# Kernel tuning notes

Hardware: AMD Instinct MI355X
Metric: run time of the kernel (lower is better)

Reference implementation:

```python
import jax, jax.numpy as jnp
import numpy as np

IGNORE = 255
THRESH = 0.7
MIN_KEPT = 100000
AUX_W = 1.0


def resize_bilinear_ac(x, oh, ow):
    # F.interpolate(..., mode='bilinear', align_corners=True); x: (b,c,h,w)
    b, c, h, w = x.shape
    ys = jnp.linspace(0.0, h - 1.0, oh)
    xs = jnp.linspace(0.0, w - 1.0, ow)
    y0 = jnp.floor(ys).astype(jnp.int32)
    x0 = jnp.floor(xs).astype(jnp.int32)
    y1 = jnp.minimum(y0 + 1, h - 1)
    x1 = jnp.minimum(x0 + 1, w - 1)
    wy = (ys - y0)[:, None]          # (oh,1) broadcasts over (b,c,oh,w)
    wx = xs - x0                     # (ow,)
    rows = x[:, :, y0, :] * (1.0 - wy) + x[:, :, y1, :] * wy   # (b,c,oh,w)
    return rows[:, :, :, x0] * (1.0 - wx) + rows[:, :, :, x1] * wx


def ohem_ce(pred, target):
    # pred: (b,c,h,w) logits, target: (b,h,w) int labels
    b, c, h, w = pred.shape
    n = b * h * w
    t = target.reshape(-1)
    valid = t != IGNORE
    t_cl = jnp.where(valid, t, 0)
    logits = pred.transpose(0, 2, 3, 1).reshape(n, c)
    logp = jax.nn.log_softmax(logits, axis=-1)
    pix = jnp.arange(n)
    logp_t = logp[pix, t_cl]
    # prob at target class; invalid pixels filled with 1 (as in masked_fill_)
    mask_prob = jnp.where(valid, jnp.exp(logp_t), 1.0)
    idx = min(n, MIN_KEPT) - 1
    thr = jnp.maximum(jnp.asarray(THRESH, pred.dtype), jnp.sort(mask_prob)[idx])
    kept = mask_prob <= thr
    final_valid = valid & kept
    nll = -logp_t
    denom = jnp.maximum(final_valid.sum(), 1).astype(pred.dtype)
    return jnp.sum(jnp.where(final_valid, nll, 0.0)) / denom


def boundary_bce(p, t):
    # p: (n,1,h,w) probs, t: (n,1,h,w) binary targets; per-sample pos/neg weights
    pos = jnp.sum(t == 1.0, axis=(1, 2, 3), keepdims=True).astype(p.dtype)
    neg = jnp.sum(t == 0.0, axis=(1, 2, 3), keepdims=True).astype(p.dtype)
    valid = pos + neg
    wgt = jnp.where(t == 1.0, neg / valid, jnp.where(t == 0.0, pos / valid, 0.0))
    logp = jnp.clip(jnp.log(p), -100.0)          # torch BCELoss clamps log at -100
    log1mp = jnp.clip(jnp.log(1.0 - p), -100.0)
    bce = -(t * logp + (1.0 - t) * log1mp)
    return jnp.mean(wgt * bce)


def setup_inputs() -> dict:
    key = jax.random.key(0)
    k1, k2, k3, k4, k5 = jax.random.split(key, 5)
    main_pred = jax.random.normal(k1, (4, 19, 64, 128), dtype=jnp.float32)
    coarse_pred = jax.random.normal(k2, (4, 19, 64, 128), dtype=jnp.float32)
    boundary_pred = jax.random.uniform(k3, (4, 1, 64, 128), dtype=jnp.float32)
    seg_gt = jax.random.randint(k4, (4, 512, 1024), 0, 19, dtype=jnp.int32)
    boundary_gt = jax.random.randint(k5, (4, 1, 512, 1024), 0, 2).astype(jnp.float32)
    return {"main_pred": main_pred, "coarse_pred": coarse_pred,
            "boundary_pred": boundary_pred, "seg_gt": seg_gt,
            "boundary_gt": boundary_gt}


def reference(main_pred, coarse_pred, boundary_pred, seg_gt, boundary_gt):
    h, w = seg_gt.shape[1], seg_gt.shape[2]
    main_up = resize_bilinear_ac(main_pred, h, w)
    loss = ohem_ce(main_up, seg_gt)
    coarse_up = resize_bilinear_ac(coarse_pred, h, w)
    loss = loss + AUX_W * ohem_ce(coarse_up, seg_gt)
    bound_up = resize_bilinear_ac(boundary_pred, h, w)
    loss = loss + boundary_bce(bound_up, boundary_gt)
    return loss
```

## Files before the change

### kernel.cpp

```cpp
#include <hip/hip_runtime.h>

#define NPX    2097152
#define NPX4   (NPX/4)
#define CH_STR 8192
#define IMG_STR 155648

#define OFF_CTL   (2ull*NPX*4)
#define CTL_HIST    0
#define CTL_BAR     24576
#define CTL_PREFIX  24578
#define CTL_KREM    24580
#define CTL_THR     24582
#define CTL_PPSUM   24584
#define CTL_PPCNT   28680
#define CTL_OPSUM   32776
#define CTL_OPCNT   33288
#define CTL_BPS     33800
#define CTL_BPC     34824

__global__ __launch_bounds__(256) void fused_pass1(
    const float* __restrict__ mp, const float* __restrict__ cp,
    const float* __restrict__ bp, const int* __restrict__ seg,
    const float* __restrict__ bg,
    float* __restrict__ probA, float* __restrict__ ppsum, unsigned* __restrict__ ppcnt,
    float* __restrict__ bps, unsigned* __restrict__ bpc, unsigned* __restrict__ bar)
{
    __shared__ float2 erow[19 * 128];
    __shared__ float rf[4]; __shared__ unsigned ru[4];
    __shared__ float rf2[4]; __shared__ unsigned ru2[4];
    int bk = blockIdx.x;
    int tid = threadIdx.x;

    if (bk == 0 && tid < 2) bar[tid] = 0u;

    if (bk < 4096) {
        int head = bk >> 11;
        int task = bk & 2047;
        int b = task >> 9;
        int y = task & 511;
        const float* pred = head ? cp : mp;

        float fy = (float)y * (63.0f / 511.0f);
        int y0 = min((int)fy, 63);
        int y1 = min(y0 + 1, 63);
        float wy = fy - (float)y0;

        const float* r0 = pred + (size_t)b * IMG_STR + y0 * 128;
        const float* r1 = pred + (size_t)b * IMG_STR + y1 * 128;
        for (int i = tid; i < 2432; i += 256) {
            int c = i >> 7, x = i & 127;
            float v0 = r0[c * CH_STR + x];
            float v1 = r1[c * CH_STR + x];
            float e = fmaf(wy, v1 - v0, v0);
            erow[c * 128 + x].x = e;
            if (x > 0)    erow[c * 128 + x - 1].y = e;
            if (x == 127) erow[c * 128 + 127].y = e;
        }
        __syncthreads();

        int xb = tid << 2;
        int P = (b * 512 + y) * 1024 + xb;
        int4 t4 = *(const int4*)(seg + P);
        int t[4] = {t4.x, t4.y, t4.z, t4.w};

        float fx0 = (float)xb * (127.0f / 1023.0f);
        int X = min((int)fx0, 126);
        float wA[4], wB[4], wC[4];
#pragma unroll
        for (int dx = 0; dx < 4; ++dx) {
            float fx = (float)(xb + dx) * (127.0f / 1023.0f);
            int x0 = min((int)fx, 127);
            float wx = fx - (float)x0;
            bool sm = (x0 == X);
            wA[dx] = sm ? (1.0f - wx) : 0.0f;
            wB[dx] = sm ? wx : (1.0f - wx);
            wC[dx] = sm ? 0.0f : wx;
        }

        float s[4] = {0.f, 0.f, 0.f, 0.f};
        for (int c = 0; c < 19; ++c) {
            float2 eA = erow[c * 128 + X];
            float2 eB = erow[c * 128 + X + 1];
#pragma unroll
            for (int dx = 0; dx < 4; ++dx) {
                float l = fmaf(eA.x, wA[dx], fmaf(eA.y, wB[dx], eB.y * wC[dx]));
                s[dx] += __expf(l);
            }
        }

        float fs = 0.f; unsigned ic = 0;
        float pr[4];
#pragma unroll
        for (int dx = 0; dx < 4; ++dx) {
            bool valid = (t[dx] != 255);
            int tc = valid ? t[dx] : 0;
            float2 eA = erow[tc * 128 + X];
            float2 eB = erow[tc * 128 + X + 1];
            float lt = fmaf(eA.x, wA[dx], fmaf(eA.y, wB[dx], eB.y * wC[dx]));
            float ls = __logf(s[dx]);
            float n  = ls - lt;
            float p  = fminf(__expf(-n), 1.0f);
            pr[dx] = valid ? p : 1.0f;
            if (valid && p <= 0.7f) { fs += n; ic++; }
        }
        *(float4*)(probA + (size_t)head * NPX + P) = make_float4(pr[0], pr[1], pr[2], pr[3]);

        for (int o = 32; o; o >>= 1) {
            fs += __shfl_down(fs, o, 64);
            ic += (unsigned)__shfl_down((int)ic, o, 64);
        }
        int wave = tid >> 6, lane = tid & 63;
        if (lane == 0) { rf[wave] = fs; ru[wave] = ic; }
        __syncthreads();
        if (tid == 0) {
            ppsum[head * 2048 + task] = rf[0] + rf[1] + rf[2] + rf[3];
            ppcnt[head * 2048 + task] = ru[0] + ru[1] + ru[2] + ru[3];
        }
    } else {
        int bb = bk - 4096;
        int b  = bb >> 7;
        int blk = bb & 127;
        float psum = 0.f, nsum = 0.f; unsigned pc = 0, nc = 0;

        for (int g = blk * 256 + tid; g < 131072; g += 128 * 256) {
            int P = g << 2;
            int y = P >> 10, xb = P & 1023;

            float fy = (float)y * (63.0f / 511.0f);
            int y0 = min((int)fy, 63);
            int y1 = min(y0 + 1, 63);
            float wy = fy - (float)y0;

            const float* r0 = bp + b * 8192 + y0 * 128;
            const float* r1 = bp + b * 8192 + y1 * 128;
            float fx0 = (float)xb * (127.0f / 1023.0f);
            int X  = min((int)fx0, 126);
            int X2 = min(X + 2, 127);
            float c0 = r0[X], c1 = r0[X + 1], c2 = r0[X2];
            float d0 = r1[X], d1 = r1[X + 1], d2 = r1[X2];
            float e0 = fmaf(wy, d0 - c0, c0);
            float e1 = fmaf(wy, d1 - c1, c1);
            float e2 = fmaf(wy, d2 - c2, c2);

            float4 t4 = *(const float4*)(bg + (size_t)b * 524288 + P);
            float tv[4] = {t4.x, t4.y, t4.z, t4.w};

#pragma unroll
            for (int dx = 0; dx < 4; ++dx) {
                float fx = (float)(xb + dx) * (127.0f / 1023.0f);
                int x0 = min((int)fx, 127);
                int x1 = min(x0 + 1, 127);
                float wx = fx - (float)x0;
                float a0 = (x0 == X)     ? e0 : e1;
                float a1 = (x1 == X + 1) ? e1 : e2;
                float p  = fmaf(wx, a1 - a0, a0);
                bool isp = (tv[dx] == 1.0f);
                bool isn = (tv[dx] == 0.0f);
                float q = isp ? p : 1.0f - p;
                float l = fmaxf(__logf(q), -100.0f);
                if (isp) { pc++; psum -= l; }
                if (isn) { nc++; nsum -= l; }
            }
        }
        for (int o = 32; o; o >>= 1) {
            psum += __shfl_down(psum, o, 64);
            nsum += __shfl_down(nsum, o, 64);
            pc   += (unsigned)__shfl_down((int)pc, o, 64);
            nc   += (unsigned)__shfl_down((int)nc, o, 64);
        }
        int wave = tid >> 6, lane = tid & 63;
        if (lane == 0) { rf[wave] = psum; rf2[wave] = nsum; ru[wave] = pc; ru2[wave] = nc; }
        __syncthreads();
        if (tid == 0) {
            bps[2 * bb]     = rf[0] + rf[1] + rf[2] + rf[3];
            bps[2 * bb + 1] = rf2[0] + rf2[1] + rf2[2] + rf2[3];
            bpc[2 * bb]     = ru[0] + ru[1] + ru[2] + ru[3];
            bpc[2 * bb + 1] = ru2[0] + ru2[1] + ru2[2] + ru2[3];
        }
    }
}

__device__ __forceinline__ void gbar(unsigned* bar, int tid) {
    __syncthreads();
    if (tid == 0) {
        unsigned g = __hip_atomic_load(&bar[1], __ATOMIC_RELAXED, __HIP_MEMORY_SCOPE_AGENT);
        unsigned t = __hip_atomic_fetch_add(&bar[0], 1u, __ATOMIC_ACQ_REL, __HIP_MEMORY_SCOPE_AGENT);
        if (t == 255u) {
            __hip_atomic_store(&bar[0], 0u, __ATOMIC_RELAXED, __HIP_MEMORY_SCOPE_AGENT);
            __hip_atomic_store(&bar[1], g + 1u, __ATOMIC_RELEASE, __HIP_MEMORY_SCOPE_AGENT);
        } else {
            while (__hip_atomic_load(&bar[1], __ATOMIC_ACQUIRE, __HIP_MEMORY_SCOPE_AGENT) == g)
                __builtin_amdgcn_s_sleep(8);
        }
    }
    __syncthreads();
}

__device__ void combine_out(int tid, float headLossSum,
                            const float* __restrict__ bps, const unsigned* __restrict__ bpc,
                            float* __restrict__ out)
{
    __shared__ float lf[256]; __shared__ unsigned lu[256];
    __shared__ float Pb[4], Nb[4]; __shared__ unsigned PCb[4], NCb[4];
    for (int b = 0; b < 4; ++b) {
        float ps = 0.f, ns = 0.f; unsigned p_c = 0, n_c = 0;
        if (tid < 128) {
            int j = b * 128 + tid;
            ps = bps[2 * j]; ns = bps[2 * j + 1];
            p_c = bpc[2 * j]; n_c = bpc[2 * j + 1];
        }
        lf[tid] = ps; lu[tid] = p_c; __syncthreads();
        for (int o = 128; o; o >>= 1) {
            if (tid < o) { lf[tid] += lf[tid + o]; lu[tid] += lu[tid + o]; }
            __syncthreads();
        }
        if (tid == 0) { Pb[b] = lf[0]; PCb[b] = lu[0]; }
        __syncthreads();
        lf[tid] = ns; lu[tid] = n_c; __syncthreads();
        for (int o = 128; o; o >>= 1) {
            if (tid < o) { lf[tid] += lf[tid + o]; lu[tid] += lu[tid + o]; }
            __syncthreads();
        }
        if (tid == 0) { Nb[b] = lf[0]; NCb[b] = lu[0]; }
        __syncthreads();
    }
    if (tid == 0) {
        float bt = 0.f;
        for (int b = 0; b < 4; ++b) {
            float pos = (float)PCb[b], neg = (float)NCb[b];
            float val = fmaxf(pos + neg, 1.f);
            bt += (neg / val) * Pb[b] + (pos / val) * Nb[b];
        }
        out[0] = headLossSum + bt / 2097152.0f;
    }
}

__global__ __launch_bounds__(256) void finish_all(
    const float* __restrict__ probA, const int* __restrict__ seg,
    const float* __restrict__ ppsum, const unsigned* __restrict__ ppcnt,
    const float* __restrict__ bps, const unsigned* __restrict__ bpc,
    unsigned* __restrict__ hist, unsigned* __restrict__ bar,
    unsigned* __restrict__ prefix, unsigned* __restrict__ krem,
    float* __restrict__ thr,
    float* __restrict__ opsum, unsigned* __restrict__ opcnt,
    float* __restrict__ out)
{
    int tid = threadIdx.x, blk = blockIdx.x;
    int wave = tid >> 6, lane = tid & 63;

    float s0 = 0.f, s1 = 0.f; unsigned c0 = 0u, c1 = 0u;
    for (int i = tid; i < 2048; i += 256) {
        s0 += ppsum[i];        c0 += ppcnt[i];
        s1 += ppsum[2048 + i]; c1 += ppcnt[2048 + i];
    }
    for (int o = 32; o; o >>= 1) {
        s0 += __shfl_down(s0, o, 64); s1 += __shfl_down(s1, o, 64);
        c0 += (unsigned)__shfl_down((int)c0, o, 64);
        c1 += (unsigned)__shfl_down((int)c1, o, 64);
    }
    __shared__ float ws0[4], ws1[4]; __shared__ unsigned wc0[4], wc1[4];
    if (lane == 0) { ws0[wave] = s0; ws1[wave] = s1; wc0[wave] = c0; wc1[wave] = c1; }
    __syncthreads();
    float S0 = ws0[0] + ws0[1] + ws0[2] + ws0[3];
    float S1 = ws1[0] + ws1[1] + ws1[2] + ws1[3];
    unsigned C0 = wc0[0] + wc0[1] + wc0[2] + wc0[3];
    unsigned C1 = wc1[0] + wc1[1] + wc1[2] + wc1[3];
    bool done0 = C0 >= 100000u, done1 = C1 >= 100000u;

    if (done0 && done1) {
        if (blk == 0)
            combine_out(tid, S0 / fmaxf((float)C0, 1.f) + S1 / fmaxf((float)C1, 1.f),
                        bps, bpc, out);
        return;
    }

    __shared__ unsigned hsh[4096];
    __shared__ unsigned cpre[257];
    unsigned doneMask = (done0 ? 1u : 0u) | (done1 ? 2u : 0u);

    for (int i = blk * 256 + tid; i < 24576; i += 65536) hist[i] = 0u;
    gbar(bar, tid);

    for (int lvl = 0; lvl < 3; ++lvl) {
        unsigned* hl = hist + lvl * 8192;
        for (int h = 0; h < 2; ++h) {
            if (doneMask & (1u << h)) continue;
            unsigned pre = (lvl == 0) ? 0u : prefix[h];
            for (int i = tid; i < 4096; i += 256) hsh[i] = 0u;
            __syncthreads();
            const float4* prob = (const float4*)(probA + (size_t)h * NPX);
            for (int i = blk * 256 + tid; i < NPX4; i += 65536) {
                float4 p = prob[i];
                unsigned u[4] = {__float_as_uint(p.x), __float_as_uint(p.y),
                                 __float_as_uint(p.z), __float_as_uint(p.w)};
#pragma unroll
                for (int k = 0; k < 4; ++k) {
                    unsigned bv = u[k];
                    if (lvl == 0)      atomicAdd(&hsh[bv >> 18], 1u);
                    else if (lvl == 1) { if ((bv >> 18) == pre) atomicAdd(&hsh[(bv >> 6) & 0xFFFu], 1u); }
                    else               { if ((bv >> 6) == pre) atomicAdd(&hsh[bv & 63u], 1u); }
                }
            }
            __syncthreads();
            for (int i = tid; i < 4096; i += 256) {
                unsigned v = hsh[i];
                if (v) atomicAdd(&hl[h * 4096 + i], v);
            }
            __syncthreads();
        }
        gbar(bar, tid);
        if (blk == 0) {
            int bins = (lvl == 2) ? 64 : 4096;
            for (int h = 0; h < 2; ++h) {
                if (doneMask & (1u << h)) continue;
                const unsigned* hh = hl + h * 4096;
                int per = (bins + 255) >> 8;
                int base = tid * per;
                unsigned ssum = 0;
                for (int i = 0; i < per; ++i) { int idx = base + i; if (idx < bins) ssum += hh[idx]; }
                cpre[tid] = ssum; __syncthreads();
                if (tid == 0) {
                    unsigned acc = 0;
                    for (int i = 0; i < 256; ++i) { unsigned v = cpre[i]; cpre[i] = acc; acc += v; }
                    cpre[256] = acc;
                }
                __syncthreads();
                unsigned K = (lvl == 0) ? 100000u : krem[h];
                unsigned my = cpre[tid], nx = cpre[tid + 1];
                if (K > 0 && my < K && K <= nx) {
                    unsigned acc = my;
                    for (int i = 0; i < per; ++i) {
                        int idx = base + i;
                        unsigned c = (idx < bins) ? hh[idx] : 0u;
                        if (acc < K && K <= acc + c) {
                            if (lvl == 0)      { prefix[h] = (unsigned)idx; krem[h] = K - acc; }
                            else if (lvl == 1) { prefix[h] = (prefix[h] << 12) | (unsigned)idx; krem[h] = K - acc; }
                            else {
                                unsigned bitsv = (prefix[h] << 6) | (unsigned)idx;
                                thr[h] = fmaxf(0.7f, __uint_as_float(bitsv));
                            }
                            break;
                        }
                        acc += c;
                    }
                }
                __syncthreads();
            }
        }
        gbar(bar, tid);
    }

    for (int h = 0; h < 2; ++h) {
        if (doneMask & (1u << h)) continue;
        float th = thr[h];
        const float4* prob = (const float4*)(probA + (size_t)h * NPX);
        const int4*   sg4  = (const int4*)seg;
        float fs = 0.f; unsigned ic = 0;
        for (int i = blk * 256 + tid; i < NPX4; i += 65536) {
            float4 p = prob[i]; int4 tt = sg4[i];
            if (tt.x != 255 && p.x <= th) { fs -= __logf(p.x); ic++; }
            if (tt.y != 255 && p.y <= th) { fs -= __logf(p.y); ic++; }
            if (tt.z != 255 && p.z <= th) { fs -= __logf(p.z); ic++; }
            if (tt.w != 255 && p.w <= th) { fs -= __logf(p.w); ic++; }
        }
        for (int o = 32; o; o >>= 1) {
            fs += __shfl_down(fs, o, 64);
            ic += (unsigned)__shfl_down((int)ic, o, 64);
        }
        __shared__ float wf[4]; __shared__ unsigned wu[4];
        if (lane == 0) { wf[wave] = fs; wu[wave] = ic; }
        __syncthreads();
        if (tid == 0) {
            opsum[h * 256 + blk] = wf[0] + wf[1] + wf[2] + wf[3];
            opcnt[h * 256 + blk] = wu[0] + wu[1] + wu[2] + wu[3];
        }
        __syncthreads();
    }
    gbar(bar, tid);
    if (blk == 0) {
        __shared__ float lf2[256]; __shared__ unsigned lu2[256];
        float hls = 0.f;
        for (int h = 0; h < 2; ++h) {
            float S; unsigned C;
            if (doneMask & (1u << h)) {
                S = h ? S1 : S0; C = h ? C1 : C0;
            } else {
                lf2[tid] = opsum[h * 256 + tid]; lu2[tid] = opcnt[h * 256 + tid];
                __syncthreads();
                for (int o = 128; o; o >>= 1) {
                    if (tid < o) { lf2[tid] += lf2[tid + o]; lu2[tid] += lu2[tid + o]; }
                    __syncthreads();
                }
                S = lf2[0]; C = lu2[0];
                __syncthreads();
            }
            hls += S / fmaxf((float)C, 1.f);
        }
        combine_out(tid, hls, bps, bpc, out);
    }
}

extern "C" void kernel_launch(void* const* d_in, const int* in_sizes, int n_in,
                              void* d_out, int out_size, void* d_ws, size_t ws_size,
                              hipStream_t stream)
{
    const float* mp  = (const float*)d_in[0];
    const float* cp  = (const float*)d_in[1];
    const float* bp  = (const float*)d_in[2];
    const int*   seg = (const int*)d_in[3];
    const float* bg  = (const float*)d_in[4];
    float* out = (float*)d_out;

    char* ws = (char*)d_ws;
    float* probA = (float*)ws;
    unsigned* ctl    = (unsigned*)(ws + OFF_CTL);
    unsigned* hist   = ctl + CTL_HIST;
    unsigned* bar    = ctl + CTL_BAR;
    unsigned* prefix = ctl + CTL_PREFIX;
    unsigned* krem   = ctl + CTL_KREM;
    float*    thr    = (float*)(ctl + CTL_THR);
    float*    ppsum  = (float*)(ctl + CTL_PPSUM);
    unsigned* ppcnt  = ctl + CTL_PPCNT;
    float*    opsum  = (float*)(ctl + CTL_OPSUM);
    unsigned* opcnt  = ctl + CTL_OPCNT;
    float*    bps    = (float*)(ctl + CTL_BPS);
    unsigned* bpc    = ctl + CTL_BPC;

    fused_pass1<<<dim3(4608), 256, 0, stream>>>(mp, cp, bp, seg, bg, probA,
                                                ppsum, ppcnt, bps, bpc, bar);
    finish_all<<<dim3(256), 256, 0, stream>>>(probA, seg, ppsum, ppcnt, bps, bpc,
                                              hist, bar, prefix, krem, thr,
                                              opsum, opcnt, out);
}
```

Measured before the change: 110.1 us.

## Process two output rows per block with 8 pixels per thread and exp2 math

Each CE block now builds two interpolated logit rows in shared memory and has each thread compute eight adjacent pixels, halving the block count and the per-block reduction overhead. Bilinear weights are prescaled by log2(e) so the softmax uses exp2/log2 directly, dropping the per-element multiply inside __expf. Launch bounds request 4 blocks per CU, and the partial-sum arrays and finish kernel are resized to 1024 entries per head. The cost is more registers per thread and double the shared memory per block, which may lower occupancy.

```diff
diff --git a/kernel.cpp b/kernel.cpp
--- a/kernel.cpp
+++ b/kernel.cpp
@@ -4,6 +4,8 @@
 #define NPX4   (NPX/4)
 #define CH_STR 8192
 #define IMG_STR 155648
+#define LOG2E  1.4426950408889634f
+#define LN2    0.6931471805599453f
 
 #define OFF_CTL   (2ull*NPX*4)
 #define CTL_HIST    0
@@ -18,14 +20,14 @@
 #define CTL_BPS     33800
 #define CTL_BPC     34824
 
-__global__ __launch_bounds__(256) void fused_pass1(
+__global__ __launch_bounds__(256, 4) void fused_pass1(
     const float* __restrict__ mp, const float* __restrict__ cp,
     const float* __restrict__ bp, const int* __restrict__ seg,
     const float* __restrict__ bg,
     float* __restrict__ probA, float* __restrict__ ppsum, unsigned* __restrict__ ppcnt,
     float* __restrict__ bps, unsigned* __restrict__ bpc, unsigned* __restrict__ bar)
 {
-    __shared__ float2 erow[19 * 128];
+    __shared__ float2 erow[2 * 19 * 128];
     __shared__ float rf[4]; __shared__ unsigned ru[4];
     __shared__ float rf2[4]; __shared__ unsigned ru2[4];
     int bk = blockIdx.x;
@@ -33,77 +35,90 @@
 
     if (bk == 0 && tid < 2) bar[tid] = 0u;
 
-    if (bk < 4096) {
-        int head = bk >> 11;
-        int task = bk & 2047;
-        int b = task >> 9;
-        int y = task & 511;
+    if (bk < 2048) {
+        int row0 = bk << 1;
+        int head = row0 >> 11;
+        int r0i  = row0 & 2047;
+        int b    = r0i >> 9;
+        int yA   = r0i & 511;
         const float* pred = head ? cp : mp;
 
-        float fy = (float)y * (63.0f / 511.0f);
-        int y0 = min((int)fy, 63);
-        int y1 = min(y0 + 1, 63);
-        float wy = fy - (float)y0;
-
-        const float* r0 = pred + (size_t)b * IMG_STR + y0 * 128;
-        const float* r1 = pred + (size_t)b * IMG_STR + y1 * 128;
-        for (int i = tid; i < 2432; i += 256) {
-            int c = i >> 7, x = i & 127;
-            float v0 = r0[c * CH_STR + x];
-            float v1 = r1[c * CH_STR + x];
-            float e = fmaf(wy, v1 - v0, v0);
-            erow[c * 128 + x].x = e;
-            if (x > 0)    erow[c * 128 + x - 1].y = e;
-            if (x == 127) erow[c * 128 + 127].y = e;
-        }
-        __syncthreads();
-
-        int xb = tid << 2;
-        int P = (b * 512 + y) * 1024 + xb;
-        int4 t4 = *(const int4*)(seg + P);
-        int t[4] = {t4.x, t4.y, t4.z, t4.w};
+        for (int r = 0; r < 2; ++r) {
+            int y = yA + r;
+            float fy = (float)y * (63.0f / 511.0f);
+            int y0 = min((int)fy, 63);
+            int y1 = min(y0 + 1, 63);
+            float wy = fy - (float)y0;
+            const float* r0 = pred + (size_t)b * IMG_STR + y0 * 128;
+            const float* r1 = pred + (size_t)b * IMG_STR + y1 * 128;
+            float2* er = erow + r * 2432;
+            for (int i = tid; i < 2432; i += 256) {
+                int c = i >> 7, x = i & 127;
+                float v0 = r0[c * CH_STR + x];
+                float v1 = r1[c * CH_STR + x];
+                float e = fmaf(wy, v1 - v0, v0);
+                er[c * 128 + x].x = e;
+                if (x > 0)    er[c * 128 + x - 1].y = e;
+                if (x == 127) er[c * 128 + 127].y = e;
+            }
+        }
+        __syncthreads();
+
+        int half = tid >> 7;
+        int xi   = tid & 127;
+        int xb   = xi << 3;
+        int y    = yA + half;
+        int P    = (b * 512 + y) * 1024 + xb;
+        const float2* er = erow + half * 2432;
+
+        int4 ta = *(const int4*)(seg + P);
+        int4 tb = *(const int4*)(seg + P + 4);
+        int t[8] = {ta.x, ta.y, ta.z, ta.w, tb.x, tb.y, tb.z, tb.w};
 
         float fx0 = (float)xb * (127.0f / 1023.0f);
         int X = min((int)fx0, 126);
-        float wA[4], wB[4], wC[4];
-#pragma unroll
-        for (int dx = 0; dx < 4; ++dx) {
+        float wA[8], wB[8], wC[8];
+#pragma unroll
+        for (int dx = 0; dx < 8; ++dx) {
             float fx = (float)(xb + dx) * (127.0f / 1023.0f);
             int x0 = min((int)fx, 127);
             float wx = fx - (float)x0;
             bool sm = (x0 == X);
-            wA[dx] = sm ? (1.0f - wx) : 0.0f;
-            wB[dx] = sm ? wx : (1.0f - wx);
-            wC[dx] = sm ? 0.0f : wx;
-        }
-
-        float s[4] = {0.f, 0.f, 0.f, 0.f};
+            wA[dx] = sm ? (1.0f - wx) * LOG2E : 0.0f;
+            wB[dx] = (sm ? wx : (1.0f - wx)) * LOG2E;
+            wC[dx] = sm ? 0.0f : wx * LOG2E;
+        }
+
+        float s[8] = {0.f, 0.f, 0.f, 0.f, 0.f, 0.f, 0.f, 0.f};
+#pragma unroll
         for (int c = 0; c < 19; ++c) {
-            float2 eA = erow[c * 128 + X];
-            float2 eB = erow[c * 128 + X + 1];
-#pragma unroll
-            for (int dx = 0; dx < 4; ++dx) {
-                float l = fmaf(eA.x, wA[dx], fmaf(eA.y, wB[dx], eB.y * wC[dx]));
-                s[dx] += __expf(l);
+            float2 eA = er[c * 128 + X];
+            float2 eB = er[c * 128 + X + 1];
+#pragma unroll
+            for (int dx = 0; dx < 8; ++dx) {
+                float l2 = fmaf(eA.x, wA[dx], fmaf(eA.y, wB[dx], eB.y * wC[dx]));
+                s[dx] += __builtin_exp2f(l2);
             }
         }
 
         float fs = 0.f; unsigned ic = 0;
-        float pr[4];
-#pragma unroll
-        for (int dx = 0; dx < 4; ++dx) {
+        float pr[8];
+#pragma unroll
+        for (int dx = 0; dx < 8; ++dx) {
             bool valid = (t[dx] != 255);
             int tc = valid ? t[dx] : 0;
-            float2 eA = erow[tc * 128 + X];
-            float2 eB = erow[tc * 128 + X + 1];
-            float lt = fmaf(eA.x, wA[dx], fmaf(eA.y, wB[dx], eB.y * wC[dx]));
-            float ls = __logf(s[dx]);
-            float n  = ls - lt;
-            float p  = fminf(__expf(-n), 1.0f);
+            float2 eA = er[tc * 128 + X];
+            float2 eB = er[tc * 128 + X + 1];
+            float lt2 = fmaf(eA.x, wA[dx], fmaf(eA.y, wB[dx], eB.y * wC[dx]));
+            float ls2 = __builtin_log2f(s[dx]);
+            float n   = LN2 * (ls2 - lt2);
+            float p   = fminf(__builtin_exp2f(lt2 - ls2), 1.0f);
             pr[dx] = valid ? p : 1.0f;
             if (valid && p <= 0.7f) { fs += n; ic++; }
         }
-        *(float4*)(probA + (size_t)head * NPX + P) = make_float4(pr[0], pr[1], pr[2], pr[3]);
+        float* pb = probA + (size_t)head * NPX + P;
+        *(float4*)pb       = make_float4(pr[0], pr[1], pr[2], pr[3]);
+        *(float4*)(pb + 4) = make_float4(pr[4], pr[5], pr[6], pr[7]);
 
         for (int o = 32; o; o >>= 1) {
             fs += __shfl_down(fs, o, 64);
@@ -113,11 +128,11 @@
         if (lane == 0) { rf[wave] = fs; ru[wave] = ic; }
         __syncthreads();
         if (tid == 0) {
-            ppsum[head * 2048 + task] = rf[0] + rf[1] + rf[2] + rf[3];
-            ppcnt[head * 2048 + task] = ru[0] + ru[1] + ru[2] + ru[3];
+            ppsum[head * 1024 + (bk & 1023)] = rf[0] + rf[1] + rf[2] + rf[3];
+            ppcnt[head * 1024 + (bk & 1023)] = ru[0] + ru[1] + ru[2] + ru[3];
         }
     } else {
-        int bb = bk - 4096;
+        int bb = bk - 2048;
         int b  = bb >> 7;
         int blk = bb & 127;
         float psum = 0.f, nsum = 0.f; unsigned pc = 0, nc = 0;
@@ -249,9 +264,9 @@
     int wave = tid >> 6, lane = tid & 63;
 
     float s0 = 0.f, s1 = 0.f; unsigned c0 = 0u, c1 = 0u;
-    for (int i = tid; i < 2048; i += 256) {
+    for (int i = tid; i < 1024; i += 256) {
         s0 += ppsum[i];        c0 += ppcnt[i];
-        s1 += ppsum[2048 + i]; c1 += ppcnt[2048 + i];
+        s1 += ppsum[1024 + i]; c1 += ppcnt[1024 + i];
     }
     for (int o = 32; o; o >>= 1) {
         s0 += __shfl_down(s0, o, 64); s1 += __shfl_down(s1, o, 64);
@@ -426,7 +441,7 @@
     float*    bps    = (float*)(ctl + CTL_BPS);
     unsigned* bpc    = ctl + CTL_BPC;
 
-    fused_pass1<<<dim3(4608), 256, 0, stream>>>(mp, cp, bp, seg, bg, probA,
+    fused_pass1<<<dim3(2560), 256, 0, stream>>>(mp, cp, bp, seg, bg, probA,
                                                 ppsum, ppcnt, bps, bpc, bar);
     finish_all<<<dim3(256), 256, 0, stream>>>(probA, seg, ppsum, ppcnt, bps, bpc,
                                               hist, bar, prefix, krem, thr,
```

Measured after the change: 115.7 us. 5.1% more time.
